# Kernel optimization log

Hardware: AMD Instinct MI355X
Metric: run time of the kernel (lower is better)

The kernel has to match this reference:

```python
import jax, jax.numpy as jnp
import numpy as np


def hsigmoid(x):
    # ReLU6(x + 3) / 6
    return jnp.clip(x + 3.0, 0.0, 6.0) / 6.0


def setup_inputs() -> dict:
    key = jax.random.key(0)
    k1, k2 = jax.random.split(key)
    B, C, H, W = 16, 256, 128, 128
    K = 7
    x = jax.random.normal(k1, (B, C, H, W), dtype=jnp.float32)
    # Kaiming-ish small init for the 2->1 7x7 conv
    conv_w = jax.random.normal(k2, (1, 2, K, K), dtype=jnp.float32) * (1.0 / np.sqrt(2 * K * K))
    conv_b = jnp.zeros((1,), dtype=jnp.float32)
    return {"x": x, "conv_w": conv_w, "conv_b": conv_b}


def reference(x, conv_w, conv_b):
    # channel-wise max and mean -> [B, 1, H, W] each
    max_x = jnp.max(x, axis=1, keepdims=True)
    avg_x = jnp.mean(x, axis=1, keepdims=True)
    out = jnp.concatenate([max_x, avg_x], axis=1)  # [B, 2, H, W]
    # 7x7 conv, stride 1, padding = k//2 (SAME for odd k)
    pad = conv_w.shape[-1] // 2
    out = jax.lax.conv_general_dilated(
        out, conv_w,
        window_strides=(1, 1),
        padding=[(pad, pad), (pad, pad)],
        dimension_numbers=("NCHW", "OIHW", "NCHW"),
    ) + conv_b[None, :, None, None]  # [B, 1, H, W]
    gate = hsigmoid(out)
    return x * gate  # broadcast over channel dim
```

## Files before the change

### kernel.cpp

```cpp
#include <hip/hip_runtime.h>
#include <math.h>

#define HW      128
#define PLANE   16384
#define CHS     256
#define BATCH   16
#define CSTRIDE 16384
#define BSTRIDE (256 * 16384)

__global__ __launch_bounds__(256) void reduce_kernel(
    const float* __restrict__ x, float* __restrict__ pmax, float* __restrict__ pavg)
{
    const int tid = threadIdx.x;
    const int sc  = tid & 63;
    const int cq  = tid >> 6;
    const int g   = blockIdx.x * 64 + sc;
    const int b   = g >> 12;
    const int sp  = (g & 4095) << 2;

    const float* xp = x + (size_t)b * BSTRIDE + sp + (size_t)(cq << 6) * CSTRIDE;

    float4 vmax = make_float4(-INFINITY, -INFINITY, -INFINITY, -INFINITY);
    float4 vsum = make_float4(0.f, 0.f, 0.f, 0.f);

    #pragma unroll 4
    for (int c = 0; c < 64; ++c) {
        const float4 v = *(const float4*)(xp + (size_t)c * CSTRIDE);
        vmax.x = fmaxf(vmax.x, v.x); vmax.y = fmaxf(vmax.y, v.y);
        vmax.z = fmaxf(vmax.z, v.z); vmax.w = fmaxf(vmax.w, v.w);
        vsum.x += v.x; vsum.y += v.y; vsum.z += v.z; vsum.w += v.w;
    }

    __shared__ float4 smax[256];
    __shared__ float4 ssum[256];
    smax[tid] = vmax;
    ssum[tid] = vsum;
    __syncthreads();

    if (tid < 64) {
        float4 m0 = smax[tid], m1 = smax[tid + 64], m2 = smax[tid + 128], m3 = smax[tid + 192];
        float4 s0 = ssum[tid], s1 = ssum[tid + 64], s2 = ssum[tid + 128], s3 = ssum[tid + 192];
        float4 m, s;
        m.x = fmaxf(fmaxf(m0.x, m1.x), fmaxf(m2.x, m3.x));
        m.y = fmaxf(fmaxf(m0.y, m1.y), fmaxf(m2.y, m3.y));
        m.z = fmaxf(fmaxf(m0.z, m1.z), fmaxf(m2.z, m3.z));
        m.w = fmaxf(fmaxf(m0.w, m1.w), fmaxf(m2.w, m3.w));
        const float inv = 1.0f / 256.0f;
        s.x = (s0.x + s1.x + s2.x + s3.x) * inv;
        s.y = (s0.y + s1.y + s2.y + s3.y) * inv;
        s.z = (s0.z + s1.z + s2.z + s3.z) * inv;
        s.w = (s0.w + s1.w + s2.w + s3.w) * inv;
        const int gg = blockIdx.x * 64 + tid;
        *(float4*)(pmax + (size_t)gg * 4) = m;
        *(float4*)(pavg + (size_t)gg * 4) = s;
    }
}

__global__ __launch_bounds__(256) void gate_mul_kernel(
    const float* __restrict__ x,
    const float* __restrict__ pmax, const float* __restrict__ pavg,
    const float* __restrict__ cw, const float* __restrict__ cb,
    float* __restrict__ out)
{
    __shared__ float sw[98];
    __shared__ __align__(16) float sgate[HW];

    const int tid = threadIdx.x;
    if (tid < 98) sw[tid] = cw[tid];
    const int b = blockIdx.x >> 7;
    const int h = blockIdx.x & 127;
    __syncthreads();

    if (tid < HW) {
        const int w = tid;
        float acc = cb[0];
        const float* pm = pmax + b * PLANE;
        const float* pa = pavg + b * PLANE;
        #pragma unroll
        for (int ky = 0; ky < 7; ++ky) {
            const int hh = h + ky - 3;
            if (hh >= 0 && hh < HW) {
                const float* prm = pm + hh * HW;
                const float* pra = pa + hh * HW;
                #pragma unroll
                for (int kx = 0; kx < 7; ++kx) {
                    const int ww = w + kx - 3;
                    if (ww >= 0 && ww < HW) {
                        acc = fmaf(sw[ky * 7 + kx],      prm[ww], acc);
                        acc = fmaf(sw[49 + ky * 7 + kx], pra[ww], acc);
                    }
                }
            }
        }
        sgate[w] = fminf(fmaxf(acc + 3.0f, 0.0f), 6.0f) * (1.0f / 6.0f);
    }
    __syncthreads();

    const int wc   = tid & 31;
    const int csub = tid >> 5;
    const float4 g4 = *(const float4*)(sgate + wc * 4);
    const size_t rowbase = (size_t)b * BSTRIDE + (size_t)h * HW + wc * 4;

    #pragma unroll 4
    for (int c = csub; c < CHS; c += 8) {
        const size_t off = rowbase + (size_t)c * CSTRIDE;
        const float4 v = *(const float4*)(x + off);
        float4 r;
        r.x = v.x * g4.x; r.y = v.y * g4.y; r.z = v.z * g4.z; r.w = v.w * g4.w;
        *(float4*)(out + off) = r;
    }
}

extern "C" void kernel_launch(void* const* d_in, const int* in_sizes, int n_in,
                              void* d_out, int out_size, void* d_ws, size_t ws_size,
                              hipStream_t stream)
{
    const float* x  = (const float*)d_in[0];
    const float* cw = (const float*)d_in[1];
    const float* cb = (const float*)d_in[2];
    float* out = (float*)d_out;

    float* pmax = (float*)d_ws;
    float* pavg = pmax + (size_t)BATCH * PLANE;

    reduce_kernel<<<1024, 256, 0, stream>>>(x, pmax, pavg);
    gate_mul_kernel<<<2048, 256, 0, stream>>>(x, pmax, pavg, cw, cb, out);
}
```

Baseline: 537.6 us.

## Process batches in chunks so x is re-read from cache, use nontemporal stores

Splits the work into four batch chunks, running reduce then gate-multiply per chunk. Each chunk's slice of x (64 MB) may then stay partly resident in the MI355X's large last-level cache for the second read. The reduce kernel now uses 32 spatial columns by 8 channel groups per block. Output stores are nontemporal so they do not evict x from cache. The cost is more kernel launches and less parallelism per launch.

```diff
diff --git a/kernel.cpp b/kernel.cpp
--- a/kernel.cpp
+++ b/kernel.cpp
@@ -7,24 +7,28 @@
 #define BATCH   16
 #define CSTRIDE 16384
 #define BSTRIDE (256 * 16384)
+#define CHUNK_B 4
+
+typedef float vf4 __attribute__((ext_vector_type(4)));
 
 __global__ __launch_bounds__(256) void reduce_kernel(
-    const float* __restrict__ x, float* __restrict__ pmax, float* __restrict__ pavg)
+    const float* __restrict__ x, float* __restrict__ pmax, float* __restrict__ pavg,
+    int b0)
 {
     const int tid = threadIdx.x;
-    const int sc  = tid & 63;
-    const int cq  = tid >> 6;
-    const int g   = blockIdx.x * 64 + sc;
-    const int b   = g >> 12;
+    const int sc  = tid & 31;
+    const int cg  = tid >> 5;
+    const int g   = blockIdx.x * 32 + sc;
+    const int b   = b0 + (g >> 12);
     const int sp  = (g & 4095) << 2;
 
-    const float* xp = x + (size_t)b * BSTRIDE + sp + (size_t)(cq << 6) * CSTRIDE;
+    const float* xp = x + (size_t)b * BSTRIDE + sp + (size_t)(cg << 5) * CSTRIDE;
 
     float4 vmax = make_float4(-INFINITY, -INFINITY, -INFINITY, -INFINITY);
     float4 vsum = make_float4(0.f, 0.f, 0.f, 0.f);
 
-    #pragma unroll 4
-    for (int c = 0; c < 64; ++c) {
+    #pragma unroll 8
+    for (int c = 0; c < 32; ++c) {
         const float4 v = *(const float4*)(xp + (size_t)c * CSTRIDE);
         vmax.x = fmaxf(vmax.x, v.x); vmax.y = fmaxf(vmax.y, v.y);
         vmax.z = fmaxf(vmax.z, v.z); vmax.w = fmaxf(vmax.w, v.w);
@@ -37,22 +41,24 @@
     ssum[tid] = vsum;
     __syncthreads();
 
-    if (tid < 64) {
-        float4 m0 = smax[tid], m1 = smax[tid + 64], m2 = smax[tid + 128], m3 = smax[tid + 192];
-        float4 s0 = ssum[tid], s1 = ssum[tid + 64], s2 = ssum[tid + 128], s3 = ssum[tid + 192];
-        float4 m, s;
-        m.x = fmaxf(fmaxf(m0.x, m1.x), fmaxf(m2.x, m3.x));
-        m.y = fmaxf(fmaxf(m0.y, m1.y), fmaxf(m2.y, m3.y));
-        m.z = fmaxf(fmaxf(m0.z, m1.z), fmaxf(m2.z, m3.z));
-        m.w = fmaxf(fmaxf(m0.w, m1.w), fmaxf(m2.w, m3.w));
+    if (tid < 32) {
+        float4 m = smax[tid];
+        float4 s = ssum[tid];
+        #pragma unroll
+        for (int j = 1; j < 8; ++j) {
+            const float4 mj = smax[tid + 32 * j];
+            const float4 sj = ssum[tid + 32 * j];
+            m.x = fmaxf(m.x, mj.x); m.y = fmaxf(m.y, mj.y);
+            m.z = fmaxf(m.z, mj.z); m.w = fmaxf(m.w, mj.w);
+            s.x += sj.x; s.y += sj.y; s.z += sj.z; s.w += sj.w;
+        }
         const float inv = 1.0f / 256.0f;
-        s.x = (s0.x + s1.x + s2.x + s3.x) * inv;
-        s.y = (s0.y + s1.y + s2.y + s3.y) * inv;
-        s.z = (s0.z + s1.z + s2.z + s3.z) * inv;
-        s.w = (s0.w + s1.w + s2.w + s3.w) * inv;
-        const int gg = blockIdx.x * 64 + tid;
-        *(float4*)(pmax + (size_t)gg * 4) = m;
-        *(float4*)(pavg + (size_t)gg * 4) = s;
+        s.x *= inv; s.y *= inv; s.z *= inv; s.w *= inv;
+        const int gg = blockIdx.x * 32 + tid;
+        const int bb = b0 + (gg >> 12);
+        const int ss = (gg & 4095) << 2;
+        *(float4*)(pmax + (size_t)bb * PLANE + ss) = m;
+        *(float4*)(pavg + (size_t)bb * PLANE + ss) = s;
     }
 }
 
@@ -60,22 +66,22 @@
     const float* __restrict__ x,
     const float* __restrict__ pmax, const float* __restrict__ pavg,
     const float* __restrict__ cw, const float* __restrict__ cb,
-    float* __restrict__ out)
+    float* __restrict__ out, int b0)
 {
     __shared__ float sw[98];
     __shared__ __align__(16) float sgate[HW];
 
     const int tid = threadIdx.x;
     if (tid < 98) sw[tid] = cw[tid];
-    const int b = blockIdx.x >> 7;
+    const int b = b0 + (blockIdx.x >> 7);
     const int h = blockIdx.x & 127;
     __syncthreads();
 
     if (tid < HW) {
         const int w = tid;
         float acc = cb[0];
-        const float* pm = pmax + b * PLANE;
-        const float* pa = pavg + b * PLANE;
+        const float* pm = pmax + (size_t)b * PLANE;
+        const float* pa = pavg + (size_t)b * PLANE;
         #pragma unroll
         for (int ky = 0; ky < 7; ++ky) {
             const int hh = h + ky - 3;
@@ -105,9 +111,9 @@
     for (int c = csub; c < CHS; c += 8) {
         const size_t off = rowbase + (size_t)c * CSTRIDE;
         const float4 v = *(const float4*)(x + off);
-        float4 r;
+        vf4 r;
         r.x = v.x * g4.x; r.y = v.y * g4.y; r.z = v.z * g4.z; r.w = v.w * g4.w;
-        *(float4*)(out + off) = r;
+        __builtin_nontemporal_store(r, (vf4*)(out + off));
     }
 }
 
@@ -123,6 +129,8 @@
     float* pmax = (float*)d_ws;
     float* pavg = pmax + (size_t)BATCH * PLANE;
 
-    reduce_kernel<<<1024, 256, 0, stream>>>(x, pmax, pavg);
-    gate_mul_kernel<<<2048, 256, 0, stream>>>(x, pmax, pavg, cw, cb, out);
+    for (int b0 = 0; b0 < BATCH; b0 += CHUNK_B) {
+        reduce_kernel<<<512, 256, 0, stream>>>(x, pmax, pavg, b0);
+        gate_mul_kernel<<<CHUNK_B * 128, 256, 0, stream>>>(x, pmax, pavg, cw, cb, out, b0);
+    }
 }
```

Result: faster. 499.2 us (-7.2%).
